# Optimization experiments

Hardware: AMD Instinct MI355X
Metric: run time of the kernel (lower is better)

The kernel has to match this reference:

```python
import math
import jax, jax.numpy as jnp
import numpy as np

N_HEAD = 16
ROPE_BASE = 10000.0


def _rope_tables(T, half, dtype):
    # build_sin_cos(seq_len, dim=head_dim//2): inv freq of length `half`
    pos = jnp.arange(T, dtype=jnp.float32)[:, None]                       # (T,1)
    inv = jnp.exp(jnp.arange(0, 2 * half, 2, dtype=jnp.float32) * (-math.log(ROPE_BASE) / (2 * half)))
    ang = pos * inv                                                        # (T, half)
    return jnp.sin(ang).astype(dtype), jnp.cos(ang).astype(dtype)


def _apply_rope(q, k, sin, cos):
    # q,k: (B,T,H,Dh); sin,cos: (T, Dh//2) -> broadcast over batch and heads
    half = q.shape[-1] // 2
    s = sin[None, :, None, :]
    c = cos[None, :, None, :]
    q1, q2 = q[..., :half], q[..., half:]
    k1, k2 = k[..., :half], k[..., half:]
    q = jnp.concatenate([q1 * c - q2 * s, q2 * c + q1 * s], axis=-1)
    k = jnp.concatenate([k1 * c - k2 * s, k2 * c + k1 * s], axis=-1)
    return q, k


def setup_inputs() -> dict:
    key = jax.random.key(0)
    k1, k2, k3 = jax.random.split(key, 3)
    B, T, C = 2, 2048, 2048
    x = jax.random.normal(k1, (B, T, C), dtype=jnp.float32)
    w_qkv = jax.random.normal(k2, (3 * C, C), dtype=jnp.float32) * (1.0 / math.sqrt(C))
    w_proj = jax.random.normal(k3, (C, C), dtype=jnp.float32) * (1.0 / math.sqrt(C))
    return {"x": x, "w_qkv": w_qkv, "w_proj": w_proj}


def reference(x, w_qkv, w_proj):
    B, T, C = x.shape
    H = N_HEAD
    Dh = C // H
    # fused QKV projection (Linear, no bias): (B,T,3C) -> (B,T,3,H,Dh)
    qkv = jnp.einsum('btc,oc->bto', x, w_qkv).reshape(B, T, 3, H, Dh)
    q, k, v = qkv[:, :, 0], qkv[:, :, 1], qkv[:, :, 2]          # (B,T,H,Dh)
    sin, cos = _rope_tables(T, Dh // 2, x.dtype)
    q, k = _apply_rope(q, k, sin, cos)
    # causal attention, scale 1/sqrt(Dh) (flash default softmax_scale=None)
    scale = 1.0 / math.sqrt(Dh)
    scores = jnp.einsum('bqhd,bkhd->bhqk', q, k) * scale        # (B,H,T,T)
    mask = jnp.tril(jnp.ones((T, T), dtype=bool))
    scores = jnp.where(mask[None, None], scores, jnp.finfo(scores.dtype).min)
    probs = jax.nn.softmax(scores, axis=-1)
    out = jnp.einsum('bhqk,bkhd->bqhd', probs, v)               # (B,T,H,Dh)
    # faithful to original: permute(0,2,1,3) then reshape_as(x)
    out = jnp.transpose(out, (0, 2, 1, 3)).reshape(B, T, C)
    return jnp.einsum('btc,oc->bto', out, w_proj)
```

## Files before the change

### kernel.cpp

```cpp
#include <hip/hip_runtime.h>
#include <hip/hip_bf16.h>

typedef __bf16 bf16_t;
typedef __bf16 bf16x8 __attribute__((ext_vector_type(8)));
typedef float f32x4 __attribute__((ext_vector_type(4)));

#define MFMA16(a, b, c) __builtin_amdgcn_mfma_f32_16x16x32_bf16(a, b, c, 0, 0, 0)

__device__ __forceinline__ void async_copy16(const void* g, void* l) {
  __builtin_amdgcn_global_load_lds(
      (const __attribute__((address_space(1))) void*)g,
      (__attribute__((address_space(3))) void*)l, 16, 0, 0);
}

__global__ void cast_f32_bf16(const float* __restrict__ in, bf16_t* __restrict__ out, int n8) {
  int stride = gridDim.x * blockDim.x;
  for (int i = blockIdx.x * blockDim.x + threadIdx.x; i < n8; i += stride) {
    const float* p = in + (size_t)i * 8;
    f32x4 a = *(const f32x4*)p;
    f32x4 b = *(const f32x4*)(p + 4);
    bf16x8 o;
    o[0] = (bf16_t)a[0]; o[1] = (bf16_t)a[1]; o[2] = (bf16_t)a[2]; o[3] = (bf16_t)a[3];
    o[4] = (bf16_t)b[0]; o[5] = (bf16_t)b[1]; o[6] = (bf16_t)b[2]; o[7] = (bf16_t)b[3];
    *(bf16x8*)(out + (size_t)i * 8) = o;
  }
}

__global__ __launch_bounds__(512, 2) void gemm_qkv(
    const bf16_t* __restrict__ A, const bf16_t* __restrict__ Bw,
    bf16_t* __restrict__ qo, bf16_t* __restrict__ ko, bf16_t* __restrict__ vto,
    int K) {
  __shared__ __align__(16) char lds[131072];
  int tid = threadIdx.x;
  int w = tid >> 6, lane = tid & 63;
  int wm = w & 1, wn = w >> 1;
  int mr = lane & 15, kg = lane >> 4;

  int orig = blockIdx.x;
  int chunk = orig & 7, i = orig >> 3;
  int by = (chunk & 3) * 4 + (i & 3);
  int bx = (chunk >> 2) * 12 + (i >> 2);
  int row0 = by * 256, col0 = bx * 256;

  size_t aoff[2], boff[2];
#pragma unroll
  for (int it = 0; it < 2; ++it) {
    int c = tid + it * 512;
    int r = c >> 2;
    int lc = (c & 3) ^ ((r >> 1) & 3);
    aoff[it] = (size_t)(row0 + r) * K + lc * 8;
    boff[it] = (size_t)(col0 + r) * K + lc * 8;
  }

  auto stageA = [&](int buf, int kt) {
    char* Ad = &lds[buf * 32768];
#pragma unroll
    for (int it = 0; it < 2; ++it)
      async_copy16(A + aoff[it] + kt * 32, Ad + (tid + it * 512) * 16);
  };
  auto stageB = [&](int buf, int kt) {
    char* Bd = &lds[buf * 32768 + 16384];
#pragma unroll
    for (int it = 0; it < 2; ++it)
      async_copy16(Bw + boff[it] + kt * 32, Bd + (tid + it * 512) * 16);
  };

  f32x4 zero = {0.f, 0.f, 0.f, 0.f};
  f32x4 acc[8][4];
#pragma unroll
  for (int mi = 0; mi < 8; ++mi)
#pragma unroll
    for (int ni = 0; ni < 4; ++ni) acc[mi][ni] = zero;

  int nt = K >> 5;
  stageA(0, 0); stageB(0, 0);
  stageA(1, 1); stageB(1, 1);
  stageA(2, 2); stageB(2, 2);
  asm volatile("s_waitcnt vmcnt(8)" ::: "memory");
  __builtin_amdgcn_sched_barrier(0);
  __builtin_amdgcn_s_barrier();
  __builtin_amdgcn_sched_barrier(0);

#pragma unroll 1
  for (int t = 0; t < nt; ++t) {
    int cur = t & 3;
    int nb = (t + 3) & 3;
    int kt3 = (t + 3 < nt) ? (t + 3) : (nt - 1);
    const char* Ab = &lds[cur * 32768];
    const char* Bb = &lds[cur * 32768 + 16384];
    bf16x8 af[8], bfr[4];
#pragma unroll
    for (int mi = 0; mi < 8; ++mi) {
      int r = wm * 128 + mi * 16 + mr;
      af[mi] = *(const bf16x8*)(Ab + r * 64 + ((kg ^ ((r >> 1) & 3)) << 4));
    }
#pragma unroll
    for (int ni = 0; ni < 4; ++ni) {
      int r = wn * 64 + ni * 16 + mr;
      bfr[ni] = *(const bf16x8*)(Bb + r * 64 + ((kg ^ ((r >> 1) & 3)) << 4));
    }
    stageA(nb, kt3);
    __builtin_amdgcn_s_setprio(1);
#pragma unroll
    for (int mi = 0; mi < 8; ++mi) acc[mi][0] = MFMA16(af[mi], bfr[0], acc[mi][0]);
#pragma unroll
    for (int mi = 0; mi < 8; ++mi) acc[mi][1] = MFMA16(af[mi], bfr[1], acc[mi][1]);
    __builtin_amdgcn_s_setprio(0);
    stageB(nb, kt3);
    __builtin_amdgcn_s_setprio(1);
#pragma unroll
    for (int mi = 0; mi < 8; ++mi) acc[mi][2] = MFMA16(af[mi], bfr[2], acc[mi][2]);
#pragma unroll
    for (int mi = 0; mi < 8; ++mi) acc[mi][3] = MFMA16(af[mi], bfr[3], acc[mi][3]);
    __builtin_amdgcn_s_setprio(0);
    asm volatile("s_waitcnt vmcnt(8)" ::: "memory");
    __builtin_amdgcn_sched_barrier(0);
    __builtin_amdgcn_s_barrier();
    __builtin_amdgcn_sched_barrier(0);
  }
  asm volatile("s_waitcnt vmcnt(0)" ::: "memory");
  __syncthreads();

  char* tb = &lds[0];
  int s = col0 >> 11;
  int h0 = (col0 >> 7) & 15;
  int b = row0 >> 11, t0 = row0 & 2047;
  if (s < 2) {
#pragma unroll
    for (int mi = 0; mi < 8; ++mi)
#pragma unroll
      for (int ni = 0; ni < 4; ++ni)
#pragma unroll
        for (int jj = 0; jj < 4; ++jj) {
          int rl = wm * 128 + mi * 16 + kg * 4 + jj;
          int cb = (wn * 64 + ni * 16 + mr) * 2;
          *(bf16_t*)(tb + rl * 512 + (cb ^ ((rl & 7) << 4))) = (bf16_t)acc[mi][ni][jj];
        }
    __syncthreads();
    int r = tid >> 1, hs = tid & 1;
    const char* rowb = tb + r * 512;
    int sz = (r & 7) << 4;
    int t = t0 + r;
    bf16_t* dst = (s == 0 ? qo : ko) + ((size_t)((b * 16 + h0 + hs) * 2048 + t)) * 128;
    float tf = (float)t;
    const float cinv = -0.20762050593046014f;
    bf16x8 vin[16];
#pragma unroll
    for (int m = 0; m < 16; ++m)
      vin[m] = *(const bf16x8*)(rowb + ((hs * 256 + m * 16) ^ sz));
#pragma unroll
    for (int m = 0; m < 8; ++m) {
      bf16x8 o1, o2;
#pragma unroll
      for (int e = 0; e < 8; ++e) {
        float ang = tf * exp2f((float)(m * 8 + e) * cinv);
        float sv = __sinf(ang), cv = __cosf(ang);
        float x1 = (float)vin[m][e], x2 = (float)vin[m + 8][e];
        o1[e] = (bf16_t)(x1 * cv - x2 * sv);
        o2[e] = (bf16_t)(x2 * cv + x1 * sv);
      }
      *(bf16x8*)(dst + m * 8) = o1;
      *(bf16x8*)(dst + 64 + m * 8) = o2;
    }
  } else {
#pragma unroll
    for (int mi = 0; mi < 8; ++mi)
#pragma unroll
      for (int ni = 0; ni < 4; ++ni)
#pragma unroll
        for (int jj = 0; jj < 4; ++jj) {
          int rl = wm * 128 + mi * 16 + kg * 4 + jj;
          int cl = wn * 64 + ni * 16 + mr;
          *(bf16_t*)(tb + cl * 512 + ((rl * 2) ^ ((cl & 7) << 4))) = (bf16_t)acc[mi][ni][jj];
        }
    __syncthreads();
    int d = tid >> 1, ts = tid & 1;
    const char* rowb = tb + d * 512;
    int sz = (d & 7) << 4;
    bf16_t* dst = vto + ((size_t)((b * 16 + h0 + (d >> 7)) * 128 + (d & 127))) * 2048 +
                  t0 + ts * 128;
#pragma unroll
    for (int m = 0; m < 16; ++m)
      *(bf16x8*)(dst + m * 8) = *(const bf16x8*)(rowb + ((ts * 256 + m * 16) ^ sz));
  }
}

template <int MODE>
__global__ __launch_bounds__(512, 2) void gemm256(
    const bf16_t* __restrict__ A, const bf16_t* __restrict__ Bw, float* __restrict__ C,
    int M, int N, int K, int nby) {
  __shared__ __align__(16) char lds[147456];
  int tid = threadIdx.x;
  int w = tid >> 6, lane = tid & 63;
  int wm = w >> 1, wn = w & 1;
  int mr = lane & 15, kg = lane >> 4;

  int nwg = gridDim.x;
  int orig = blockIdx.x;
  int wgid = (orig & 7) * (nwg >> 3) + (orig >> 3);
  int by = wgid % nby, bx = wgid / nby;
  int row0 = by * 256, col0 = bx * 128;

  size_t aoff[4], boff[2];
#pragma unroll
  for (int it = 0; it < 4; ++it) {
    int c = tid + it * 512;
    int r = c >> 3;
    int chs = (c & 7) ^ (r & 7);
    aoff[it] = (size_t)(row0 + r) * K + chs * 8;
  }
#pragma unroll
  for (int it = 0; it < 2; ++it) {
    int c = tid + it * 512;
    int r = c >> 3;
    int chs = (c & 7) ^ (r & 7);
    boff[it] = (size_t)(col0 + r) * K + chs * 8;
  }

  auto stageA = [&](int buf, int kt, int half) {
    char* Ad = &lds[buf * 49152];
#pragma unroll
    for (int it = half * 2; it < half * 2 + 2; ++it)
      async_copy16(A + aoff[it] + kt * 64, Ad + (tid + it * 512) * 16);
  };
  auto stageB = [&](int buf, int kt) {
    char* Bd = &lds[buf * 49152 + 32768];
#pragma unroll
    for (int it = 0; it < 2; ++it)
      async_copy16(Bw + boff[it] + kt * 64, Bd + (tid + it * 512) * 16);
  };

  f32x4 zero = {0.f, 0.f, 0.f, 0.f};
  f32x4 acc[4][4];
#pragma unroll
  for (int mi = 0; mi < 4; ++mi)
#pragma unroll
    for (int ni = 0; ni < 4; ++ni) acc[mi][ni] = zero;

  int nt = K >> 6;
  stageA(0, 0, 0); stageA(0, 0, 1); stageB(0, 0);
  stageA(1, 1, 0); stageA(1, 1, 1); stageB(1, 1);
  asm volatile("s_waitcnt vmcnt(6)" ::: "memory");
  __builtin_amdgcn_sched_barrier(0);
  __builtin_amdgcn_s_barrier();
  __builtin_amdgcn_sched_barrier(0);

#pragma unroll 1
  for (int t = 0; t < nt; ++t) {
    int cur = t % 3;
    int nxt = (t + 2) % 3;
    int kt2 = (t + 2 < nt) ? (t + 2) : t;
    const char* Ab = &lds[cur * 49152];
    const char* Bb = &lds[cur * 49152 + 32768];
    bf16x8 af[4][2], bfr[4][2];
#pragma unroll
    for (int mi = 0; mi < 4; ++mi) {
      int row = wm * 64 + mi * 16 + mr;
      const char* rb = Ab + row * 128;
      int sz = (row & 7) << 4;
      af[mi][0] = *(const bf16x8*)(rb + ((kg * 16) ^ sz));
      af[mi][1] = *(const bf16x8*)(rb + ((64 + kg * 16) ^ sz));
    }
#pragma unroll
    for (int ni = 0; ni < 4; ++ni) {
      int row = wn * 64 + ni * 16 + mr;
      const char* rb = Bb + row * 128;
      int sz = (row & 7) << 4;
      bfr[ni][0] = *(const bf16x8*)(rb + ((kg * 16) ^ sz));
      bfr[ni][1] = *(const bf16x8*)(rb + ((64 + kg * 16) ^ sz));
    }
    stageA(nxt, kt2, 0);
    __builtin_amdgcn_s_setprio(1);
#pragma unroll
    for (int mi = 0; mi < 4; ++mi) {
      acc[mi][0] = MFMA16(af[mi][0], bfr[0][0], acc[mi][0]);
      acc[mi][0] = MFMA16(af[mi][1], bfr[0][1], acc[mi][0]);
    }
    __builtin_amdgcn_s_setprio(0);
    stageA(nxt, kt2, 1);
    __builtin_amdgcn_s_setprio(1);
#pragma unroll
    for (int mi = 0; mi < 4; ++mi) {
      acc[mi][1] = MFMA16(af[mi][0], bfr[1][0], acc[mi][1]);
      acc[mi][1] = MFMA16(af[mi][1], bfr[1][1], acc[mi][1]);
    }
    __builtin_amdgcn_s_setprio(0);
    stageB(nxt, kt2);
    __builtin_amdgcn_s_setprio(1);
#pragma unroll
    for (int mi = 0; mi < 4; ++mi) {
      acc[mi][2] = MFMA16(af[mi][0], bfr[2][0], acc[mi][2]);
      acc[mi][2] = MFMA16(af[mi][1], bfr[2][1], acc[mi][2]);
      acc[mi][3] = MFMA16(af[mi][0], bfr[3][0], acc[mi][3]);
      acc[mi][3] = MFMA16(af[mi][1], bfr[3][1], acc[mi][3]);
    }
    __builtin_amdgcn_s_setprio(0);
    asm volatile("s_waitcnt vmcnt(6)" ::: "memory");
    __builtin_amdgcn_sched_barrier(0);
    __builtin_amdgcn_s_barrier();
    __builtin_amdgcn_sched_barrier(0);
  }
  asm volatile("s_waitcnt vmcnt(0)" ::: "memory");
  __syncthreads();

#pragma unroll
  for (int mi = 0; mi < 4; ++mi)
#pragma unroll
    for (int ni = 0; ni < 4; ++ni)
#pragma unroll
      for (int jj = 0; jj < 4; ++jj) {
        int row = row0 + wm * 64 + mi * 16 + kg * 4 + jj;
        int col = col0 + wn * 64 + ni * 16 + mr;
        C[(size_t)row * N + col] = acc[mi][ni][jj];
      }
}

__global__ __launch_bounds__(256) void attn_kernel(
    const bf16_t* __restrict__ qg, const bf16_t* __restrict__ kgl,
    const bf16_t* __restrict__ vtg, bf16_t* __restrict__ og) {
  __shared__ __align__(16) bf16_t Ks[2][64 * 128];
  __shared__ __align__(16) bf16_t Vs[2][128 * 64];
  __shared__ __align__(16) bf16_t plds[4][1024];
  const int T = 2048;
  int tid = threadIdx.x;
  int w = tid >> 6, lane = tid & 63;
  int mr = lane & 15, kg = lane >> 4;
  int swz = (mr & 7) << 4;

  int L = blockIdx.y * 16 + blockIdx.x;
  int role = (L & 7) * 64 + (L >> 3);
  int bx = role & 15, bh = role >> 4;

  const bf16_t* Q = qg + (size_t)bh * T * 128;
  const bf16_t* K = kgl + (size_t)bh * T * 128;
  const bf16_t* Vt = vtg + (size_t)bh * 128 * T;

  int sb = tid * 16;
  int krl = sb >> 8;
  int kc = (sb & 255) ^ ((krl & 7) << 4);
  size_t ksrc = (size_t)krl * 128 + (kc >> 1);
  int vdl = sb >> 7;
  int vc = (sb & 127) ^ ((vdl & 7) << 4);
  size_t vsrc = (size_t)vdl * 2048 + (vc >> 1);

  auto stage = [&](int buf, int kb) {
#pragma unroll
    for (int it = 0; it < 4; ++it)
      async_copy16(K + (size_t)(kb + it * 16) * 128 + ksrc, &Ks[buf][it * 2048 + tid * 8]);
#pragma unroll
    for (int it = 0; it < 4; ++it)
      async_copy16(Vt + (size_t)it * 65536 + kb + vsrc, &Vs[buf][it * 2048 + tid * 8]);
  };

  const float cscale = 0.12751744f;
  f32x4 zero = {0.f, 0.f, 0.f, 0.f};
  bf16_t* P = &plds[w][0];
  int b = bh >> 4, h = bh & 15;

#pragma unroll 1
  for (int ph = 0; ph < 2; ++ph) {
    int qb = ph ? bx : (31 - bx);
    int qr0 = qb * 64 + w * 16;
    bf16x8 qf[4];
#pragma unroll
    for (int db = 0; db < 4; ++db)
      qf[db] = *(const bf16x8*)(Q + (size_t)(qr0 + mr) * 128 + db * 32 + kg * 8);

    f32x4 acc[8];
#pragma unroll
    for (int d2 = 0; d2 < 8; ++d2) acc[d2] = zero;
    float mrun[4] = {-1e30f, -1e30f, -1e30f, -1e30f};
    float lrun[4] = {0.f, 0.f, 0.f, 0.f};

    int nj = qb + 1;
    __syncthreads();
    stage(0, 0);
    int cur = 0;
#pragma unroll 1
    for (int j = 0; j < nj; ++j) {
      __syncthreads();
      if (j + 1 < nj) stage(cur ^ 1, (j + 1) * 64);
      const char* KsB = (const char*)&Ks[cur][0];
      const char* VsB = (const char*)&Vs[cur][0];
      int kb = j * 64;
      f32x4 s[4];
#pragma unroll
      for (int ntl = 0; ntl < 4; ++ntl) {
        s[ntl] = zero;
        int rowb = (ntl * 16 + mr) * 256;
#pragma unroll
        for (int db = 0; db < 4; ++db) {
          bf16x8 kf = *(const bf16x8*)(KsB + rowb + ((db * 64 + kg * 16) ^ swz));
          s[ntl] = MFMA16(qf[db], kf, s[ntl]);
        }
      }
      float pvv[4][4];
      float tmax[4] = {-3e38f, -3e38f, -3e38f, -3e38f};
      bool diag = (j == qb);
#pragma unroll
      for (int ntl = 0; ntl < 4; ++ntl)
#pragma unroll
        for (int jj = 0; jj < 4; ++jj) {
          float v = s[ntl][jj] * cscale;
          if (diag && (kb + ntl * 16 + mr) > (qr0 + kg * 4 + jj)) v = -1e30f;
          pvv[ntl][jj] = v;
          tmax[jj] = fmaxf(tmax[jj], v);
        }
#pragma unroll
      for (int m = 1; m < 16; m <<= 1)
#pragma unroll
        for (int jj = 0; jj < 4; ++jj)
          tmax[jj] = fmaxf(tmax[jj], __shfl_xor(tmax[jj], m, 64));
      bool ok = true;
#pragma unroll
      for (int jj = 0; jj < 4; ++jj) ok &= (tmax[jj] <= mrun[jj] + 8.0f);
      if (!__all(ok)) {
#pragma unroll
        for (int jj = 0; jj < 4; ++jj) {
          float mn = fmaxf(mrun[jj], tmax[jj]);
          float corr = __builtin_amdgcn_exp2f(mrun[jj] - mn);
          mrun[jj] = mn;
          lrun[jj] *= corr;
#pragma unroll
          for (int d2 = 0; d2 < 8; ++d2) acc[d2][jj] *= corr;
        }
      }
      float rs[4] = {0.f, 0.f, 0.f, 0.f};
#pragma unroll
      for (int ntl = 0; ntl < 4; ++ntl)
#pragma unroll
        for (int jj = 0; jj < 4; ++jj) {
          float p = __builtin_amdgcn_exp2f(pvv[ntl][jj] - mrun[jj]);
          pvv[ntl][jj] = p;
          rs[jj] += p;
        }
#pragma unroll
      for (int m = 1; m < 16; m <<= 1)
#pragma unroll
        for (int jj = 0; jj < 4; ++jj) rs[jj] += __shfl_xor(rs[jj], m, 64);
#pragma unroll
      for (int jj = 0; jj < 4; ++jj) lrun[jj] += rs[jj];
#pragma unroll
      for (int ntl = 0; ntl < 4; ++ntl)
#pragma unroll
        for (int jj = 0; jj < 4; ++jj) {
          int rr = kg * 4 + jj;
          int cbyte = (mr + ntl * 16) * 2;
          *(bf16_t*)((char*)P + rr * 128 + (cbyte ^ ((rr & 7) << 4))) = (bf16_t)pvv[ntl][jj];
        }
#pragma unroll
      for (int ks = 0; ks < 2; ++ks) {
        int cb = (ks * 32 + kg * 8) * 2;
        bf16x8 pa = *(const bf16x8*)((const char*)P + mr * 128 + (cb ^ ((mr & 7) << 4)));
#pragma unroll
        for (int d2 = 0; d2 < 8; ++d2) {
          bf16x8 vf = *(const bf16x8*)(VsB + (d2 * 16 + mr) * 128 + ((ks * 64 + kg * 16) ^ swz));
          acc[d2] = MFMA16(pa, vf, acc[d2]);
        }
      }
      cur ^= 1;
    }
#pragma unroll
    for (int jj = 0; jj < 4; ++jj) {
      float invl = 1.0f / lrun[jj];
      int t = qr0 + kg * 4 + jj;
      size_t row = (size_t)b * 2048 + h * 128 + (t >> 4);
      bf16_t* orow = og + row * 2048 + (t & 15) * 128;
#pragma unroll
      for (int d2 = 0; d2 < 8; ++d2)
        orow[d2 * 16 + mr] = (bf16_t)(acc[d2][jj] * invl);
    }
  }
}

extern "C" void kernel_launch(void* const* d_in, const int* in_sizes, int n_in,
                              void* d_out, int out_size, void* d_ws, size_t ws_size,
                              hipStream_t stream) {
  const float* x = (const float*)d_in[0];
  const float* wqkv = (const float*)d_in[1];
  const float* wproj = (const float*)d_in[2];
  float* out = (float*)d_out;
  char* ws = (char*)d_ws;

  const size_t OFF_WQKV = 16777216;
  const size_t OFF_Q = 41943040;
  const size_t OFF_K = 58720256;
  const size_t OFF_VT = 75497472;

  bf16_t* xb = (bf16_t*)(ws);
  bf16_t* wqkvb = (bf16_t*)(ws + OFF_WQKV);
  bf16_t* g_q = (bf16_t*)(ws + OFF_Q);
  bf16_t* g_k = (bf16_t*)(ws + OFF_K);
  bf16_t* g_vt = (bf16_t*)(ws + OFF_VT);
  bf16_t* g_att = (bf16_t*)(ws);
  bf16_t* wprojb = (bf16_t*)(ws + OFF_WQKV);

  cast_f32_bf16<<<2048, 256, 0, stream>>>(x, xb, 8388608 / 8);
  cast_f32_bf16<<<2048, 256, 0, stream>>>(wqkv, wqkvb, 12582912 / 8);
  gemm_qkv<<<384, 512, 0, stream>>>(xb, wqkvb, g_q, g_k, g_vt, 2048);
  cast_f32_bf16<<<2048, 256, 0, stream>>>(wproj, wprojb, 4194304 / 8);
  attn_kernel<<<dim3(16, 32), 256, 0, stream>>>(g_q, g_k, g_vt, g_att);
  gemm256<0><<<256, 512, 0, stream>>>(g_att, wprojb, out, 4096, 2048, 2048, 16);
}
```

Baseline: 277.5 us.

## Restructure QKV GEMM main loop into double-buffered BK=64 four-phase pipeline

The QKV projection GEMM moves from a 4-stage BK=32 LDS ring to a double-buffered BK=64 layout with an 8-chunk XOR swizzle. Each k-step is split into four phases that interleave A-fragment loads, partial async staging of the next tile and MFMA bursts, with barriers between phases. The goal is fewer loop iterations, wider K per LDS read, and finer overlap of global-to-LDS copies with compute. The cost is shallower prefetch depth and more barriers per iteration. The gemm256 template parameter is also dropped as cleanup.

```diff
diff --git a/kernel.cpp b/kernel.cpp
--- a/kernel.cpp
+++ b/kernel.cpp
@@ -42,27 +42,24 @@
   int bx = (chunk >> 2) * 12 + (i >> 2);
   int row0 = by * 256, col0 = bx * 256;
 
-  size_t aoff[2], boff[2];
-#pragma unroll
-  for (int it = 0; it < 2; ++it) {
-    int c = tid + it * 512;
-    int r = c >> 2;
-    int lc = (c & 3) ^ ((r >> 1) & 3);
-    aoff[it] = (size_t)(row0 + r) * K + lc * 8;
-    boff[it] = (size_t)(col0 + r) * K + lc * 8;
-  }
-
-  auto stageA = [&](int buf, int kt) {
-    char* Ad = &lds[buf * 32768];
-#pragma unroll
-    for (int it = 0; it < 2; ++it)
-      async_copy16(A + aoff[it] + kt * 32, Ad + (tid + it * 512) * 16);
+  int lr = tid >> 3, ch = (tid & 7) ^ (lr & 7);
+  size_t aoff[4], boff[4];
+#pragma unroll
+  for (int g = 0; g < 4; ++g) {
+    int gr = g * 32 + (lr & 31) + (lr >> 5) * 128;
+    aoff[g] = (size_t)(row0 + gr) * K + ch * 8;
+  }
+#pragma unroll
+  for (int p = 0; p < 4; ++p) {
+    int gr = (lr >> 4) * 64 + p * 16 + (lr & 15);
+    boff[p] = (size_t)(col0 + gr) * K + ch * 8;
+  }
+
+  auto stgA = [&](int q, int g, int kt) {
+    async_copy16(A + aoff[g] + kt * 64, lds + q * 65536 + g * 8192 + tid * 16);
   };
-  auto stageB = [&](int buf, int kt) {
-    char* Bd = &lds[buf * 32768 + 16384];
-#pragma unroll
-    for (int it = 0; it < 2; ++it)
-      async_copy16(Bw + boff[it] + kt * 32, Bd + (tid + it * 512) * 16);
+  auto stgB = [&](int q, int p, int kt) {
+    async_copy16(Bw + boff[p] + kt * 64, lds + q * 65536 + 32768 + p * 8192 + tid * 16);
   };
 
   f32x4 zero = {0.f, 0.f, 0.f, 0.f};
@@ -72,51 +69,62 @@
 #pragma unroll
     for (int ni = 0; ni < 4; ++ni) acc[mi][ni] = zero;
 
-  int nt = K >> 5;
-  stageA(0, 0); stageB(0, 0);
-  stageA(1, 1); stageB(1, 1);
-  stageA(2, 2); stageB(2, 2);
-  asm volatile("s_waitcnt vmcnt(8)" ::: "memory");
+  int nt = K >> 6;
+
+  stgB(0, 0, 0); stgB(0, 1, 0); stgB(0, 2, 0); stgB(0, 3, 0);
+  stgA(0, 0, 0); stgA(0, 1, 0); stgA(0, 2, 0); stgA(0, 3, 0);
+  asm volatile("s_waitcnt vmcnt(0)" ::: "memory");
   __builtin_amdgcn_sched_barrier(0);
   __builtin_amdgcn_s_barrier();
   __builtin_amdgcn_sched_barrier(0);
 
 #pragma unroll 1
   for (int t = 0; t < nt; ++t) {
-    int cur = t & 3;
-    int nb = (t + 3) & 3;
-    int kt3 = (t + 3 < nt) ? (t + 3) : (nt - 1);
-    const char* Ab = &lds[cur * 32768];
-    const char* Bb = &lds[cur * 32768 + 16384];
-    bf16x8 af[8], bfr[4];
-#pragma unroll
-    for (int mi = 0; mi < 8; ++mi) {
-      int r = wm * 128 + mi * 16 + mr;
-      af[mi] = *(const bf16x8*)(Ab + r * 64 + ((kg ^ ((r >> 1) & 3)) << 4));
-    }
+    int q = t & 1, qn = q ^ 1;
+    int kt = (t + 1 < nt) ? (t + 1) : t;
+    const char* Ab = lds + q * 65536;
+    const char* Bb = Ab + 32768;
+    bf16x8 bf[4][2];
+
+#define QKV_PHASE(MI0, STG0, STG1, WAIT)                                        \
+    {                                                                           \
+      int r0 = ((MI0) >> 1) * 64 + wm * 32 + mr;                                \
+      int r1 = r0 + 16;                                                         \
+      bf16x8 a00 = *(const bf16x8*)(Ab + r0 * 128 + ((kg * 16) ^ ((r0 & 7) << 4)));      \
+      bf16x8 a01 = *(const bf16x8*)(Ab + r0 * 128 + ((64 + kg * 16) ^ ((r0 & 7) << 4))); \
+      bf16x8 a10 = *(const bf16x8*)(Ab + r1 * 128 + ((kg * 16) ^ ((r1 & 7) << 4)));      \
+      bf16x8 a11 = *(const bf16x8*)(Ab + r1 * 128 + ((64 + kg * 16) ^ ((r1 & 7) << 4))); \
+      STG0; STG1;                                                               \
+      __builtin_amdgcn_sched_barrier(0);                                        \
+      asm volatile("s_waitcnt vmcnt(" #WAIT ")" ::: "memory");                  \
+      __builtin_amdgcn_s_barrier();                                             \
+      asm volatile("s_waitcnt lgkmcnt(0)" ::: "memory");                        \
+      __builtin_amdgcn_sched_barrier(0);                                        \
+      __builtin_amdgcn_s_setprio(1);                                            \
+      _Pragma("unroll")                                                         \
+      for (int ni = 0; ni < 4; ++ni) {                                          \
+        acc[MI0][ni] = MFMA16(a00, bf[ni][0], acc[MI0][ni]);                    \
+        acc[MI0][ni] = MFMA16(a01, bf[ni][1], acc[MI0][ni]);                    \
+        acc[(MI0) + 1][ni] = MFMA16(a10, bf[ni][0], acc[(MI0) + 1][ni]);        \
+        acc[(MI0) + 1][ni] = MFMA16(a11, bf[ni][1], acc[(MI0) + 1][ni]);        \
+      }                                                                         \
+      __builtin_amdgcn_s_setprio(0);                                            \
+      __builtin_amdgcn_sched_barrier(0);                                        \
+      __builtin_amdgcn_s_barrier();                                             \
+      __builtin_amdgcn_sched_barrier(0);                                        \
+    }
+
 #pragma unroll
     for (int ni = 0; ni < 4; ++ni) {
-      int r = wn * 64 + ni * 16 + mr;
-      bfr[ni] = *(const bf16x8*)(Bb + r * 64 + ((kg ^ ((r >> 1) & 3)) << 4));
-    }
-    stageA(nb, kt3);
-    __builtin_amdgcn_s_setprio(1);
-#pragma unroll
-    for (int mi = 0; mi < 8; ++mi) acc[mi][0] = MFMA16(af[mi], bfr[0], acc[mi][0]);
-#pragma unroll
-    for (int mi = 0; mi < 8; ++mi) acc[mi][1] = MFMA16(af[mi], bfr[1], acc[mi][1]);
-    __builtin_amdgcn_s_setprio(0);
-    stageB(nb, kt3);
-    __builtin_amdgcn_s_setprio(1);
-#pragma unroll
-    for (int mi = 0; mi < 8; ++mi) acc[mi][2] = MFMA16(af[mi], bfr[2], acc[mi][2]);
-#pragma unroll
-    for (int mi = 0; mi < 8; ++mi) acc[mi][3] = MFMA16(af[mi], bfr[3], acc[mi][3]);
-    __builtin_amdgcn_s_setprio(0);
-    asm volatile("s_waitcnt vmcnt(8)" ::: "memory");
-    __builtin_amdgcn_sched_barrier(0);
-    __builtin_amdgcn_s_barrier();
-    __builtin_amdgcn_sched_barrier(0);
+      int rb = ni * 64 + wn * 16 + mr;
+      bf[ni][0] = *(const bf16x8*)(Bb + rb * 128 + ((kg * 16) ^ ((rb & 7) << 4)));
+      bf[ni][1] = *(const bf16x8*)(Bb + rb * 128 + ((64 + kg * 16) ^ ((rb & 7) << 4)));
+    }
+    QKV_PHASE(0, stgB(qn, 0, kt), stgB(qn, 1, kt), 4)
+    QKV_PHASE(2, stgB(qn, 2, kt), stgB(qn, 3, kt), 5)
+    QKV_PHASE(4, stgA(qn, 0, kt), stgA(qn, 1, kt), 6)
+    QKV_PHASE(6, stgA(qn, 2, kt), stgA(qn, 3, kt), 3)
+#undef QKV_PHASE
   }
   asm volatile("s_waitcnt vmcnt(0)" ::: "memory");
   __syncthreads();
@@ -185,7 +193,6 @@
   }
 }
 
-template <int MODE>
 __global__ __launch_bounds__(512, 2) void gemm256(
     const bf16_t* __restrict__ A, const bf16_t* __restrict__ Bw, float* __restrict__ C,
     int M, int N, int K, int nby) {
@@ -500,5 +507,5 @@
   gemm_qkv<<<384, 512, 0, stream>>>(xb, wqkvb, g_q, g_k, g_vt, 2048);
   cast_f32_bf16<<<2048, 256, 0, stream>>>(wproj, wprojb, 4194304 / 8);
   attn_kernel<<<dim3(16, 32), 256, 0, stream>>>(g_q, g_k, g_vt, g_att);
-  gemm256<0><<<256, 512, 0, stream>>>(g_att, wprojb, out, 4096, 2048, 2048, 16);
+  gemm256<<<256, 512, 0, stream>>>(g_att, wprojb, out, 4096, 2048, 2048, 16);
 }
```

Measured after the change: 276.5 us. About the same (-0.3%).
